# Optimization experiments

Hardware: AMD Instinct MI355X
Metric: run time of the kernel (lower is better)

The kernel has to match this reference:

```python
import jax, jax.numpy as jnp
import numpy as np

INPUT_DIM = 1024
EMBED_DIMS = 128


def setup_inputs() -> dict:
    key = jax.random.key(0)
    ks = jax.random.split(key, 7)
    s_in = 1.0 / np.sqrt(INPUT_DIM)
    x = jax.random.normal(ks[0], (4, 4096, INPUT_DIM), dtype=jnp.float32)
    Wq = jax.random.uniform(ks[1], (INPUT_DIM, EMBED_DIMS), jnp.float32, -s_in, s_in)
    bq = jax.random.uniform(ks[2], (EMBED_DIMS,), jnp.float32, -s_in, s_in)
    Wk = jax.random.uniform(ks[3], (INPUT_DIM, EMBED_DIMS), jnp.float32, -s_in, s_in)
    bk = jax.random.uniform(ks[4], (EMBED_DIMS,), jnp.float32, -s_in, s_in)
    Wv = jax.random.uniform(ks[5], (INPUT_DIM, EMBED_DIMS), jnp.float32, -s_in, s_in)
    bv = jax.random.uniform(ks[6], (EMBED_DIMS,), jnp.float32, -s_in, s_in)
    return {"x": x, "Wq": Wq, "bq": bq, "Wk": Wk, "bk": bk, "Wv": Wv, "bv": bv}


def reference(x, Wq, bq, Wk, bk, Wv, bv):
    # x: [B, L, C]
    Q = jnp.einsum('blc,cd->bld', x, Wq) + bq  # [B, L, D]
    K = jnp.einsum('blc,cd->bld', x, Wk) + bk
    V = jnp.einsum('blc,cd->bld', x, Wv) + bv
    d_k = Q.shape[-1]
    scores = jnp.einsum('bld,bmd->blm', Q, K) / jnp.sqrt(jnp.float32(d_k))  # [B, L, L]
    attn = jax.nn.softmax(scores, axis=-1)
    return jnp.einsum('blm,bmd->bld', attn, V)  # [B, L, D]
```

## Files before the change

kernel.cpp:

```cpp
#include <hip/hip_runtime.h>
#include <stdint.h>

typedef __bf16 bf16;
typedef __bf16 bf16x8 __attribute__((ext_vector_type(8)));
typedef __bf16 bf16x4 __attribute__((ext_vector_type(4)));
typedef _Float16 f16;
typedef f16 f16x8 __attribute__((ext_vector_type(8)));
typedef f16 f16x4 __attribute__((ext_vector_type(4)));
typedef float f32x4 __attribute__((ext_vector_type(4)));
typedef float f32x16 __attribute__((ext_vector_type(16)));
typedef uint32_t u32x4 __attribute__((ext_vector_type(4)));

#define LQ    16384
#define CDIM  1024
#define DDIM  128
#define NSPLIT 4
#define QS 0.12751741f

static __device__ __forceinline__ uint32_t pkrtz(float a, float b) {
  return __builtin_bit_cast(uint32_t, __builtin_amdgcn_cvt_pkrtz(a, b));
}

static __device__ __forceinline__ void lds_barrier() {
  asm volatile("s_waitcnt lgkmcnt(0)" ::: "memory");
  __builtin_amdgcn_s_barrier();
}

__global__ void prep_kernel(const float* __restrict__ Wq, const float* __restrict__ Wk,
                            const float* __restrict__ Wv, const float* __restrict__ bq,
                            const float* __restrict__ bk, const float* __restrict__ bv,
                            bf16* __restrict__ Wt, float* __restrict__ bias_all) {
  int idx = blockIdx.x * 256 + threadIdx.x;
  int p = idx >> 17;
  int rem = idx & 131071;
  int k = rem >> 7, n = rem & 127;
  const float* W = (p == 0) ? Wq : (p == 1) ? Wk : Wv;
  float s = (p == 0) ? QS : 1.0f;
  Wt[(size_t)(p * 128 + n) * CDIM + k] = (bf16)(W[rem] * s);
  if (idx < 384) {
    int pp = idx >> 7, nn = idx & 127;
    const float* b = (pp == 0) ? bq : (pp == 1) ? bk : bv;
    bias_all[idx] = b[nn] * ((pp == 0) ? QS : 1.0f);
  }
}

__global__ __launch_bounds__(512, 1) void qkv_gemm(
    const float* __restrict__ x, const bf16* __restrict__ Wt,
    const float* __restrict__ bias_all,
    bf16* __restrict__ Qw, bf16* __restrict__ Kw, f16* __restrict__ Vtw) {
  __shared__ bf16 As[2][64 * 64];
  __shared__ bf16 Bs[2][384 * 64];
  const int t = threadIdx.x;
  const int w = t >> 6;
  const int lane = t & 63;
  const int l31 = lane & 31;
  const int hi = lane >> 5;
  const int m0 = blockIdx.x * 64;
  const int m_off = (w & 1) * 32;
  const int n_off = ((w >> 1) & 3) * 32;

  const f32x16 z16 = {0.f,0.f,0.f,0.f,0.f,0.f,0.f,0.f,0.f,0.f,0.f,0.f,0.f,0.f,0.f,0.f};
  f32x16 acc[3];
  acc[0] = z16; acc[1] = z16; acc[2] = z16;

  const int srow = t >> 3;
  const int g = t & 7;
  const int sgoff = (g ^ (srow & 7)) * 8;
  const int scol = g * 8;

  float4 xa[2];
  bf16x8 wa[6];
  {
    const float* p = &x[(size_t)(m0 + srow) * CDIM + scol];
    xa[0] = *(const float4*)p;
    xa[1] = *(const float4*)(p + 4);
  }
#pragma unroll
  for (int c = 0; c < 6; c++)
    wa[c] = *(const bf16x8*)&Wt[(size_t)(c * 64 + srow) * CDIM + scol];

  for (int kc = 0; kc < 16; kc++) {
    bf16* Ab = As[kc & 1];
    bf16* Bb = Bs[kc & 1];
    {
      bf16x8 v;
      v[0] = (bf16)xa[0].x; v[1] = (bf16)xa[0].y;
      v[2] = (bf16)xa[0].z; v[3] = (bf16)xa[0].w;
      v[4] = (bf16)xa[1].x; v[5] = (bf16)xa[1].y;
      v[6] = (bf16)xa[1].z; v[7] = (bf16)xa[1].w;
      *(bf16x8*)&Ab[srow * 64 + sgoff] = v;
    }
#pragma unroll
    for (int c = 0; c < 6; c++)
      *(bf16x8*)&Bb[(c * 64 + srow) * 64 + sgoff] = wa[c];

    const int kn = (kc < 15 ? kc + 1 : 15) * 64;
    {
      const float* p = &x[(size_t)(m0 + srow) * CDIM + kn + scol];
      xa[0] = *(const float4*)p;
      xa[1] = *(const float4*)(p + 4);
    }
#pragma unroll
    for (int c = 0; c < 6; c++)
      wa[c] = *(const bf16x8*)&Wt[(size_t)(c * 64 + srow) * CDIM + kn + scol];

    lds_barrier();

#pragma unroll
    for (int ks = 0; ks < 4; ks++) {
      const int rg = ((ks * 2 + hi) ^ (l31 & 7)) * 8;
      bf16x8 af = *(const bf16x8*)&Ab[(m_off + l31) * 64 + rg];
#pragma unroll
      for (int p = 0; p < 3; p++) {
        bf16x8 bfr = *(const bf16x8*)&Bb[(p * 128 + n_off + l31) * 64 + rg];
        acc[p] = __builtin_amdgcn_mfma_f32_32x32x16_bf16(af, bfr, acc[p], 0, 0, 0);
      }
    }
  }

  const int n = n_off + l31;
#pragma unroll
  for (int p = 0; p < 3; p++) {
    const float bias = bias_all[p * 128 + n];
    if (p < 2) {
      bf16* outp = (p == 0) ? Qw : Kw;
#pragma unroll
      for (int r = 0; r < 16; r++) {
        int m = m0 + m_off + (r & 3) + 8 * (r >> 2) + 4 * hi;
        outp[(size_t)m * DDIM + n] = (bf16)(acc[p][r] + bias);
      }
    } else {
#pragma unroll
      for (int gq = 0; gq < 4; gq++) {
        int mbase = m0 + m_off + 8 * gq + 4 * hi;
        f16x4 pv;
#pragma unroll
        for (int r = 0; r < 4; r++) pv[r] = (f16)(acc[p][gq * 4 + r] + bias);
        *(f16x4*)&Vtw[(size_t)n * LQ + mbase] = pv;
      }
    }
  }
}

__global__ __launch_bounds__(256, 2) void flash_kernel(
    const bf16* __restrict__ Qw, const bf16* __restrict__ Kw, const f16* __restrict__ Vtw,
    bf16* __restrict__ Opb, float* __restrict__ lp) {
  __shared__ bf16 Kl[2][64 * 136];
  __shared__ f16  Vl[2][128 * 72];

  const int t = threadIdx.x;
  const int w = t >> 6;
  const int lane = t & 63;
  const int l31 = lane & 31;
  const int hi = lane >> 5;
  const int lin = blockIdx.y * 128 + blockIdx.x;
  const int logical = ((lin & 7) << 6) + (lin >> 3);
  const int qb = logical & 127;
  const int sp = logical >> 7;
  const int batch = qb >> 5;
  const int q0w = qb * 128 + w * 32;
  const int kv_base = batch * 4096 + sp * 1024;

  bf16x8 qf[8];
#pragma unroll
  for (int ks = 0; ks < 8; ks++)
    qf[ks] = *(const bf16x8*)&Qw[(size_t)(q0w + l31) * DDIM + ks * 16 + hi * 8];

  const f32x16 z16 = {0.f,0.f,0.f,0.f,0.f,0.f,0.f,0.f,0.f,0.f,0.f,0.f,0.f,0.f,0.f,0.f};
  f32x16 o[4];
  o[0] = z16; o[1] = z16; o[2] = z16; o[3] = z16;
  f32x16 liacc = z16;

  f16x8 ones;
#pragma unroll
  for (int i = 0; i < 8; i++) ones[i] = (f16)1.f;

  const int kr = t >> 4;
  const int kcol = (t & 15) << 3;
  const int vr = t >> 3;
  const int vcol = (t & 7) << 3;

  bf16x8 ka[4];
  f16x8 va[4];
#pragma unroll
  for (int c = 0; c < 4; c++)
    ka[c] = *(const bf16x8*)&Kw[(size_t)(kv_base + c * 16 + kr) * DDIM + kcol];
#pragma unroll
  for (int c = 0; c < 4; c++)
    va[c] = *(const f16x8*)&Vtw[(size_t)(c * 32 + vr) * LQ + kv_base + vcol];

  for (int tile = 0; tile < 16; tile++) {
    bf16* Kb = Kl[tile & 1];
    f16*  Vb = Vl[tile & 1];
#pragma unroll
    for (int c = 0; c < 4; c++)
      *(bf16x8*)&Kb[(c * 16 + kr) * 136 + kcol] = ka[c];
#pragma unroll
    for (int c = 0; c < 4; c++)
      *(f16x8*)&Vb[(c * 32 + vr) * 72 + vcol] = va[c];

    const int kvn = kv_base + (tile < 15 ? tile + 1 : 15) * 64;
#pragma unroll
    for (int c = 0; c < 4; c++)
      ka[c] = *(const bf16x8*)&Kw[(size_t)(kvn + c * 16 + kr) * DDIM + kcol];
#pragma unroll
    for (int c = 0; c < 4; c++)
      va[c] = *(const f16x8*)&Vtw[(size_t)(c * 32 + vr) * LQ + kvn + vcol];

    lds_barrier();

    f32x16 sv0 = z16, sv1 = z16;
    __builtin_amdgcn_s_setprio(1);
#pragma unroll
    for (int ks = 0; ks < 8; ks++) {
      bf16x8 kf0 = *(const bf16x8*)&Kb[l31 * 136 + ks * 16 + hi * 8];
      bf16x8 kf1 = *(const bf16x8*)&Kb[(32 + l31) * 136 + ks * 16 + hi * 8];
      sv0 = __builtin_amdgcn_mfma_f32_32x32x16_bf16(kf0, qf[ks], sv0, 0, 0, 0);
      sv1 = __builtin_amdgcn_mfma_f32_32x32x16_bf16(kf1, qf[ks], sv1, 0, 0, 0);
    }
    __builtin_amdgcn_s_setprio(0);

#pragma unroll
    for (int r = 0; r < 16; r++) {
      sv0[r] = __builtin_amdgcn_exp2f(sv0[r]);
      sv1[r] = __builtin_amdgcn_exp2f(sv1[r]);
    }

#pragma unroll
    for (int mk = 0; mk < 2; mk++) {
      const f32x16 s = mk ? sv1 : sv0;
#pragma unroll
      for (int h = 0; h < 2; h++) {
        const int b = h * 8;
        uint32_t a0 = pkrtz(s[b + 0], s[b + 1]);
        uint32_t a1 = pkrtz(s[b + 2], s[b + 3]);
        uint32_t a2 = pkrtz(s[b + 4], s[b + 5]);
        uint32_t a3 = pkrtz(s[b + 6], s[b + 7]);
        asm("v_permlane32_swap_b32 %0, %1" : "+v"(a0), "+v"(a2));
        asm("v_permlane32_swap_b32 %0, %1" : "+v"(a1), "+v"(a3));
        u32x4 aw; aw.x = a0; aw.y = a1; aw.z = a2; aw.w = a3;
        f16x8 pa = __builtin_bit_cast(f16x8, aw);
        __builtin_amdgcn_s_setprio(1);
#pragma unroll
        for (int dt = 0; dt < 4; dt++) {
          f16x8 vf = *(const f16x8*)&Vb[(dt * 32 + l31) * 72 + mk * 32 + h * 16 + hi * 8];
          o[dt] = __builtin_amdgcn_mfma_f32_32x32x16_f16(pa, vf, o[dt], 0, 0, 0);
        }
        liacc = __builtin_amdgcn_mfma_f32_32x32x16_f16(pa, ones, liacc, 0, 0, 0);
        __builtin_amdgcn_s_setprio(0);
      }
    }
  }

  const size_t po = (size_t)sp * LQ * DDIM;
#pragma unroll
  for (int dt = 0; dt < 4; dt++)
#pragma unroll
    for (int r = 0; r < 16; r++) {
      int q = q0w + (r & 3) + 8 * (r >> 2) + 4 * hi;
      Opb[po + (size_t)q * DDIM + dt * 32 + l31] = (bf16)o[dt][r];
    }
  if (l31 == 0) {
#pragma unroll
    for (int r = 0; r < 16; r++)
      lp[(size_t)sp * LQ + q0w + (r & 3) + 8 * (r >> 2) + 4 * hi] = liacc[r];
  }
}

__global__ void combine_kernel(const bf16* __restrict__ Opb, const float* __restrict__ lp,
                               float* __restrict__ out) {
  int idx = blockIdx.x * 256 + threadIdx.x;
  int q = idx >> 5;
  int d = (idx & 31) * 4;
  float lsum = 0.f;
  float acc[4] = {0.f, 0.f, 0.f, 0.f};
#pragma unroll
  for (int sp = 0; sp < NSPLIT; sp++) {
    lsum += lp[(size_t)sp * LQ + q];
    bf16x4 ov = *(const bf16x4*)&Opb[(size_t)sp * LQ * DDIM + (size_t)q * DDIM + d];
#pragma unroll
    for (int j = 0; j < 4; j++) acc[j] += (float)ov[j];
  }
  float inv = 1.0f / lsum;
  float4 r;
  r.x = acc[0] * inv; r.y = acc[1] * inv; r.z = acc[2] * inv; r.w = acc[3] * inv;
  *(float4*)&out[(size_t)q * DDIM + d] = r;
}

extern "C" void kernel_launch(void* const* d_in, const int* in_sizes, int n_in,
                              void* d_out, int out_size, void* d_ws, size_t ws_size,
                              hipStream_t stream) {
  const float* x  = (const float*)d_in[0];
  const float* Wq = (const float*)d_in[1];
  const float* bq = (const float*)d_in[2];
  const float* Wk = (const float*)d_in[3];
  const float* bk = (const float*)d_in[4];
  const float* Wv = (const float*)d_in[5];
  const float* bv = (const float*)d_in[6];
  char* ws = (char*)d_ws;
  bf16* Qw   = (bf16*)(ws);
  bf16* Kw   = (bf16*)(ws + ((size_t)4 << 20));
  f16*  Vtw  = (f16*)(ws + ((size_t)8 << 20));
  bf16* Wt   = (bf16*)(ws + ((size_t)12 << 20));
  float* bias_all = (float*)(ws + ((size_t)12 << 20) + 786432);
  bf16* Opb  = (bf16*)(ws + ((size_t)13 << 20));
  float* lpp = (float*)(ws + ((size_t)29 << 20));
  float* out = (float*)d_out;

  prep_kernel<<<1536, 256, 0, stream>>>(Wq, Wk, Wv, bq, bk, bv, Wt, bias_all);
  qkv_gemm<<<256, 512, 0, stream>>>(x, Wt, bias_all, Qw, Kw, Vtw);
  flash_kernel<<<dim3(128, NSPLIT), 256, 0, stream>>>(Qw, Kw, Vtw, Opb, lpp);
  combine_kernel<<<2048, 256, 0, stream>>>(Opb, lpp, out);
}
```

Baseline: 171.2 us.

## Software-pipeline QK^T of next tile with PV of current tile

```diff
diff --git a/kernel.cpp b/kernel.cpp
--- a/kernel.cpp
+++ b/kernel.cpp
@@ -182,6 +182,8 @@
 
   bf16x8 ka[4];
   f16x8 va[4];
+  f16x8 pa[4];
+
 #pragma unroll
   for (int c = 0; c < 4; c++)
     ka[c] = *(const bf16x8*)&Kw[(size_t)(kv_base + c * 16 + kr) * DDIM + kcol];
@@ -189,9 +191,62 @@
   for (int c = 0; c < 4; c++)
     va[c] = *(const f16x8*)&Vtw[(size_t)(c * 32 + vr) * LQ + kv_base + vcol];
 
-  for (int tile = 0; tile < 16; tile++) {
-    bf16* Kb = Kl[tile & 1];
-    f16*  Vb = Vl[tile & 1];
+#pragma unroll
+  for (int c = 0; c < 4; c++)
+    *(bf16x8*)&Kl[0][(c * 16 + kr) * 136 + kcol] = ka[c];
+#pragma unroll
+  for (int c = 0; c < 4; c++)
+    *(f16x8*)&Vl[0][(c * 32 + vr) * 72 + vcol] = va[c];
+
+#pragma unroll
+  for (int c = 0; c < 4; c++)
+    ka[c] = *(const bf16x8*)&Kw[(size_t)(kv_base + 64 + c * 16 + kr) * DDIM + kcol];
+#pragma unroll
+  for (int c = 0; c < 4; c++)
+    va[c] = *(const f16x8*)&Vtw[(size_t)(c * 32 + vr) * LQ + kv_base + 64 + vcol];
+
+  lds_barrier();
+
+  f32x16 sv0 = z16, sv1 = z16;
+  __builtin_amdgcn_s_setprio(1);
+#pragma unroll
+  for (int ks = 0; ks < 8; ks++) {
+    bf16x8 kf0 = *(const bf16x8*)&Kl[0][l31 * 136 + ks * 16 + hi * 8];
+    bf16x8 kf1 = *(const bf16x8*)&Kl[0][(32 + l31) * 136 + ks * 16 + hi * 8];
+    sv0 = __builtin_amdgcn_mfma_f32_32x32x16_bf16(kf0, qf[ks], sv0, 0, 0, 0);
+    sv1 = __builtin_amdgcn_mfma_f32_32x32x16_bf16(kf1, qf[ks], sv1, 0, 0, 0);
+  }
+  __builtin_amdgcn_s_setprio(0);
+#pragma unroll
+  for (int r = 0; r < 16; r++) {
+    sv0[r] = __builtin_amdgcn_exp2f(sv0[r]);
+    sv1[r] = __builtin_amdgcn_exp2f(sv1[r]);
+  }
+#pragma unroll
+  for (int sl = 0; sl < 4; sl++) {
+    const int b = (sl & 1) * 8;
+    float s0 = (sl >> 1) ? sv1[b + 0] : sv0[b + 0];
+    float s1 = (sl >> 1) ? sv1[b + 1] : sv0[b + 1];
+    float s2 = (sl >> 1) ? sv1[b + 2] : sv0[b + 2];
+    float s3 = (sl >> 1) ? sv1[b + 3] : sv0[b + 3];
+    float s4 = (sl >> 1) ? sv1[b + 4] : sv0[b + 4];
+    float s5 = (sl >> 1) ? sv1[b + 5] : sv0[b + 5];
+    float s6 = (sl >> 1) ? sv1[b + 6] : sv0[b + 6];
+    float s7 = (sl >> 1) ? sv1[b + 7] : sv0[b + 7];
+    uint32_t a0 = pkrtz(s0, s1);
+    uint32_t a1 = pkrtz(s2, s3);
+    uint32_t a2 = pkrtz(s4, s5);
+    uint32_t a3 = pkrtz(s6, s7);
+    asm("v_permlane32_swap_b32 %0, %1" : "+v"(a0), "+v"(a2));
+    asm("v_permlane32_swap_b32 %0, %1" : "+v"(a1), "+v"(a3));
+    u32x4 aw; aw.x = a0; aw.y = a1; aw.z = a2; aw.w = a3;
+    pa[sl] = __builtin_bit_cast(f16x8, aw);
+  }
+
+  for (int tile = 0; tile < 15; tile++) {
+    bf16* Kb = Kl[(tile + 1) & 1];
+    f16*  Vb = Vl[(tile + 1) & 1];
+    f16*  Vp = Vl[tile & 1];
 #pragma unroll
     for (int c = 0; c < 4; c++)
       *(bf16x8*)&Kb[(c * 16 + kr) * 136 + kcol] = ka[c];
@@ -199,7 +254,7 @@
     for (int c = 0; c < 4; c++)
       *(f16x8*)&Vb[(c * 32 + vr) * 72 + vcol] = va[c];
 
-    const int kvn = kv_base + (tile < 15 ? tile + 1 : 15) * 64;
+    const int kvn = kv_base + (tile < 14 ? tile + 2 : 15) * 64;
 #pragma unroll
     for (int c = 0; c < 4; c++)
       ka[c] = *(const bf16x8*)&Kw[(size_t)(kvn + c * 16 + kr) * DDIM + kcol];
@@ -209,14 +264,25 @@
 
     lds_barrier();
 
-    f32x16 sv0 = z16, sv1 = z16;
+    sv0 = z16; sv1 = z16;
     __builtin_amdgcn_s_setprio(1);
 #pragma unroll
-    for (int ks = 0; ks < 8; ks++) {
-      bf16x8 kf0 = *(const bf16x8*)&Kb[l31 * 136 + ks * 16 + hi * 8];
-      bf16x8 kf1 = *(const bf16x8*)&Kb[(32 + l31) * 136 + ks * 16 + hi * 8];
-      sv0 = __builtin_amdgcn_mfma_f32_32x32x16_bf16(kf0, qf[ks], sv0, 0, 0, 0);
-      sv1 = __builtin_amdgcn_mfma_f32_32x32x16_bf16(kf1, qf[ks], sv1, 0, 0, 0);
+    for (int i = 0; i < 4; i++) {
+      bf16x8 kf0a = *(const bf16x8*)&Kb[l31 * 136 + (2 * i) * 16 + hi * 8];
+      bf16x8 kf1a = *(const bf16x8*)&Kb[(32 + l31) * 136 + (2 * i) * 16 + hi * 8];
+      bf16x8 kf0b = *(const bf16x8*)&Kb[l31 * 136 + (2 * i + 1) * 16 + hi * 8];
+      bf16x8 kf1b = *(const bf16x8*)&Kb[(32 + l31) * 136 + (2 * i + 1) * 16 + hi * 8];
+      sv0 = __builtin_amdgcn_mfma_f32_32x32x16_bf16(kf0a, qf[2 * i], sv0, 0, 0, 0);
+      sv1 = __builtin_amdgcn_mfma_f32_32x32x16_bf16(kf1a, qf[2 * i], sv1, 0, 0, 0);
+      const int koff = (i >> 1) * 32 + (i & 1) * 16 + hi * 8;
+#pragma unroll
+      for (int dt = 0; dt < 4; dt++) {
+        f16x8 vf = *(const f16x8*)&Vp[(dt * 32 + l31) * 72 + koff];
+        o[dt] = __builtin_amdgcn_mfma_f32_32x32x16_f16(pa[i], vf, o[dt], 0, 0, 0);
+      }
+      liacc = __builtin_amdgcn_mfma_f32_32x32x16_f16(pa[i], ones, liacc, 0, 0, 0);
+      sv0 = __builtin_amdgcn_mfma_f32_32x32x16_bf16(kf0b, qf[2 * i + 1], sv0, 0, 0, 0);
+      sv1 = __builtin_amdgcn_mfma_f32_32x32x16_bf16(kf1b, qf[2 * i + 1], sv1, 0, 0, 0);
     }
     __builtin_amdgcn_s_setprio(0);
 
@@ -225,31 +291,42 @@
       sv0[r] = __builtin_amdgcn_exp2f(sv0[r]);
       sv1[r] = __builtin_amdgcn_exp2f(sv1[r]);
     }
-
-#pragma unroll
-    for (int mk = 0; mk < 2; mk++) {
-      const f32x16 s = mk ? sv1 : sv0;
-#pragma unroll
-      for (int h = 0; h < 2; h++) {
-        const int b = h * 8;
-        uint32_t a0 = pkrtz(s[b + 0], s[b + 1]);
-        uint32_t a1 = pkrtz(s[b + 2], s[b + 3]);
-        uint32_t a2 = pkrtz(s[b + 4], s[b + 5]);
-        uint32_t a3 = pkrtz(s[b + 6], s[b + 7]);
-        asm("v_permlane32_swap_b32 %0, %1" : "+v"(a0), "+v"(a2));
-        asm("v_permlane32_swap_b32 %0, %1" : "+v"(a1), "+v"(a3));
-        u32x4 aw; aw.x = a0; aw.y = a1; aw.z = a2; aw.w = a3;
-        f16x8 pa = __builtin_bit_cast(f16x8, aw);
-        __builtin_amdgcn_s_setprio(1);
-#pragma unroll
-        for (int dt = 0; dt < 4; dt++) {
-          f16x8 vf = *(const f16x8*)&Vb[(dt * 32 + l31) * 72 + mk * 32 + h * 16 + hi * 8];
-          o[dt] = __builtin_amdgcn_mfma_f32_32x32x16_f16(pa, vf, o[dt], 0, 0, 0);
-        }
-        liacc = __builtin_amdgcn_mfma_f32_32x32x16_f16(pa, ones, liacc, 0, 0, 0);
-        __builtin_amdgcn_s_setprio(0);
-      }
-    }
+#pragma unroll
+    for (int sl = 0; sl < 4; sl++) {
+      const int b = (sl & 1) * 8;
+      float s0 = (sl >> 1) ? sv1[b + 0] : sv0[b + 0];
+      float s1 = (sl >> 1) ? sv1[b + 1] : sv0[b + 1];
+      float s2 = (sl >> 1) ? sv1[b + 2] : sv0[b + 2];
+      float s3 = (sl >> 1) ? sv1[b + 3] : sv0[b + 3];
+      float s4 = (sl >> 1) ? sv1[b + 4] : sv0[b + 4];
+      float s5 = (sl >> 1) ? sv1[b + 5] : sv0[b + 5];
+      float s6 = (sl >> 1) ? sv1[b + 6] : sv0[b + 6];
+      float s7 = (sl >> 1) ? sv1[b + 7] : sv0[b + 7];
+      uint32_t a0 = pkrtz(s0, s1);
+      uint32_t a1 = pkrtz(s2, s3);
+      uint32_t a2 = pkrtz(s4, s5);
+      uint32_t a3 = pkrtz(s6, s7);
+      asm("v_permlane32_swap_b32 %0, %1" : "+v"(a0), "+v"(a2));
+      asm("v_permlane32_swap_b32 %0, %1" : "+v"(a1), "+v"(a3));
+      u32x4 aw; aw.x = a0; aw.y = a1; aw.z = a2; aw.w = a3;
+      pa[sl] = __builtin_bit_cast(f16x8, aw);
+    }
+  }
+
+  {
+    f16* Vp = Vl[15 & 1];
+    __builtin_amdgcn_s_setprio(1);
+#pragma unroll
+    for (int i = 0; i < 4; i++) {
+      const int koff = (i >> 1) * 32 + (i & 1) * 16 + hi * 8;
+#pragma unroll
+      for (int dt = 0; dt < 4; dt++) {
+        f16x8 vf = *(const f16x8*)&Vp[(dt * 32 + l31) * 72 + koff];
+        o[dt] = __builtin_amdgcn_mfma_f32_32x32x16_f16(pa[i], vf, o[dt], 0, 0, 0);
+      }
+      liacc = __builtin_amdgcn_mfma_f32_32x32x16_f16(pa[i], ones, liacc, 0, 0, 0);
+    }
+    __builtin_amdgcn_s_setprio(0);
   }
 
   const size_t po = (size_t)sp * LQ * DDIM;
```

After: 169.3 us. About the same (-1.1%).
